# Performance work log

Hardware: AMD Instinct MI355X
Metric: run time of the kernel (lower is better)

## Reference

```python
import jax, jax.numpy as jnp
import numpy as np

TOKENS = 50257
DIMS = 1024
BATCH = 4
SEQ = 4096


def setup_inputs() -> dict:
    key = jax.random.key(0)
    k1, k2 = jax.random.split(key)
    x = jax.random.randint(k1, (BATCH, SEQ), 0, TOKENS, dtype=jnp.int64 if jax.config.jax_enable_x64 else jnp.int32)
    # nn.Linear(tokens, dims).weight has shape [dims, tokens]
    W = jax.random.normal(k2, (DIMS, TOKENS), dtype=jnp.float32) * (1.0 / np.sqrt(TOKENS))
    return {"x": x, "W": W}


def reference(x, W):
    # Original: out = one_hot(x, tokens) @ W.T  (Linear with no bias).
    # one_hot @ W.T is mathematically a row gather from W.T: out[b, s, :] = W[:, x[b, s]].
    # We compute the identical result without materializing the [B, S, tokens] one-hot.
    return jnp.take(W.T, x, axis=0)  # [B, S, dims]
```

## Files before the change

kernel.cpp:

```cpp
#include <hip/hip_runtime.h>


#define DIMS    1024
#define TOKENS  50257
#define WBITS   6
#define WSIZE   64
#define NW      ((TOKENS + WSIZE - 1) / WSIZE)

__global__ void zero_cnt(int* cnt) {
    int t = threadIdx.x;
    if (t < NW) cnt[t] = 0;
}

__global__ void hist_kernel(const int* __restrict__ x, int* __restrict__ cnt, int n) {
    int i = blockIdx.x * blockDim.x + threadIdx.x;
    if (i < n) atomicAdd(&cnt[x[i] >> WBITS], 1);
}

__global__ __launch_bounds__(1024) void scan_kernel(const int* __restrict__ cnt,
                                                    int* __restrict__ offs,
                                                    int* __restrict__ cursor) {
    __shared__ int s[1024];
    int t = threadIdx.x;
    int v = (t < NW) ? cnt[t] : 0;
    s[t] = v;
    __syncthreads();
    for (int off = 1; off < 1024; off <<= 1) {
        int u = (t >= off) ? s[t - off] : 0;
        __syncthreads();
        s[t] += u;
        __syncthreads();
    }
    if (t < NW) {
        offs[t + 1] = s[t];
        cursor[t]   = s[t] - v;
    }
    if (t == 0) offs[0] = 0;
}

__global__ void scatter_kernel(const int* __restrict__ x, int* __restrict__ cursor,
                               int* __restrict__ sorted_pos, int* __restrict__ sorted_tok,
                               int n) {
    int i = blockIdx.x * blockDim.x + threadIdx.x;
    if (i < n) {
        int tok = x[i];
        int p = atomicAdd(&cursor[tok >> WBITS], 1);
        sorted_pos[p] = i;
        sorted_tok[p] = tok;
    }
}

__global__ __launch_bounds__(256) void embed_main(
    const float* __restrict__ W,
    const int* __restrict__ offs,
    const int* __restrict__ sorted_pos,
    const int* __restrict__ sorted_tok,
    float* __restrict__ out)
{
    __shared__ float tile[WSIZE * 65];
    const int w     = blockIdx.x;
    const int dbase = blockIdx.y * WSIZE;
    const int t  = threadIdx.x;
    const int c  = t & 63;
    const int rq = t >> 6;

    const int id0 = w * WSIZE;
    const int id  = id0 + c;
    const bool ok = (id < TOKENS);

    #pragma unroll
    for (int i = 0; i < 16; ++i) {
        int r = i * 4 + rq;
        float v = ok ? W[(size_t)(dbase + r) * TOKENS + id] : 0.0f;
        tile[r * 65 + c] = v;
    }
    __syncthreads();

    const int beg = offs[w];
    const int n   = offs[w + 1] - beg;
    const int d  = t & 63;
    const int jo = t >> 6;
    for (int jb = 0; jb < n; jb += 4) {
        int j = jb + jo;
        if (j < n) {
            int tok = sorted_tok[beg + j];
            int p   = sorted_pos[beg + j];
            float v = tile[d * 65 + (tok - id0)];
            out[(size_t)p * DIMS + dbase + d] = v;
        }
    }
}

extern "C" void kernel_launch(void* const* d_in, const int* in_sizes, int n_in,
                              void* d_out, int out_size, void* d_ws, size_t ws_size,
                              hipStream_t stream) {
    const int*   x = (const int*)d_in[0];
    const float* W = (const float*)d_in[1];
    float*     out = (float*)d_out;

    const int n = in_sizes[0];

    int* cnt        = (int*)d_ws;
    int* offs       = cnt + NW;
    int* cursor     = offs + (NW + 1);
    int* sorted_pos = cursor + NW;
    int* sorted_tok = sorted_pos + n;

    zero_cnt<<<1, 1024, 0, stream>>>(cnt);
    hist_kernel<<<(n + 255) / 256, 256, 0, stream>>>(x, cnt, n);
    scan_kernel<<<1, 1024, 0, stream>>>(cnt, offs, cursor);
    scatter_kernel<<<(n + 255) / 256, 256, 0, stream>>>(x, cursor, sorted_pos, sorted_tok, n);

    dim3 grid(NW, DIMS / WSIZE);
    embed_main<<<grid, 256, 0, stream>>>(W, offs, sorted_pos, sorted_tok, out);
}
```

Baseline: 345.2 us.

## Fuse bucket sort into one block kernel and widen embed tiles to 128

Replaces the four preprocessing launches (zero, histogram, scan, scatter) with a single 1024-thread block that stages x in LDS, bins with shared atomics, scans and scatters. Sorted entries are packed as position<<16|token in one 32-bit word. The transpose tile grows from 64x64 to 128x128 with 512 threads per block, which halves the number of column windows. Packing assumes positions fit in 16 bits; n=16384 does fit. The single-block sort serialises work on one CU, and the larger tile raises LDS use to about 66KB per block, which may lower occupancy.

```diff
diff --git a/kernel.cpp b/kernel.cpp
--- a/kernel.cpp
+++ b/kernel.cpp
@@ -3,90 +3,92 @@
 
 #define DIMS    1024
 #define TOKENS  50257
-#define WBITS   6
-#define WSIZE   64
+#define WBITS   7
+#define WSIZE   128
 #define NW      ((TOKENS + WSIZE - 1) / WSIZE)
+#define PAD     129
+#define NMAX    16384
 
-__global__ void zero_cnt(int* cnt) {
-    int t = threadIdx.x;
-    if (t < NW) cnt[t] = 0;
-}
+__global__ __launch_bounds__(1024) void sort_kernel(
+    const int* __restrict__ x, int n,
+    int* __restrict__ offs,
+    unsigned int* __restrict__ sorted)
+{
+    __shared__ int xl[NMAX];
+    __shared__ int bins[NW];
+    __shared__ int scanbuf[512];
+    __shared__ int cursor[NW];
+    const int t = threadIdx.x;
 
-__global__ void hist_kernel(const int* __restrict__ x, int* __restrict__ cnt, int n) {
-    int i = blockIdx.x * blockDim.x + threadIdx.x;
-    if (i < n) atomicAdd(&cnt[x[i] >> WBITS], 1);
-}
+    const bool fits = (n <= NMAX);
+    if (fits) for (int i = t; i < n; i += 1024) xl[i] = x[i];
+    if (t < NW) bins[t] = 0;
+    __syncthreads();
+    const int* xs = fits ? xl : x;
 
-__global__ __launch_bounds__(1024) void scan_kernel(const int* __restrict__ cnt,
-                                                    int* __restrict__ offs,
-                                                    int* __restrict__ cursor) {
-    __shared__ int s[1024];
-    int t = threadIdx.x;
-    int v = (t < NW) ? cnt[t] : 0;
-    s[t] = v;
+    for (int i = t; i < n; i += 1024)
+        atomicAdd(&bins[xs[i] >> WBITS], 1);
     __syncthreads();
-    for (int off = 1; off < 1024; off <<= 1) {
-        int u = (t >= off) ? s[t - off] : 0;
+
+    if (t < 512) scanbuf[t] = (t < NW) ? bins[t] : 0;
+    __syncthreads();
+    for (int off = 1; off < 512; off <<= 1) {
+        int u = 0;
+        if (t < 512 && t >= off) u = scanbuf[t - off];
         __syncthreads();
-        s[t] += u;
+        if (t < 512) scanbuf[t] += u;
         __syncthreads();
     }
     if (t < NW) {
-        offs[t + 1] = s[t];
-        cursor[t]   = s[t] - v;
+        offs[t + 1] = scanbuf[t];
+        cursor[t]   = scanbuf[t] - bins[t];
     }
     if (t == 0) offs[0] = 0;
-}
+    __syncthreads();
 
-__global__ void scatter_kernel(const int* __restrict__ x, int* __restrict__ cursor,
-                               int* __restrict__ sorted_pos, int* __restrict__ sorted_tok,
-                               int n) {
-    int i = blockIdx.x * blockDim.x + threadIdx.x;
-    if (i < n) {
-        int tok = x[i];
+    for (int i = t; i < n; i += 1024) {
+        int tok = xs[i];
         int p = atomicAdd(&cursor[tok >> WBITS], 1);
-        sorted_pos[p] = i;
-        sorted_tok[p] = tok;
+        sorted[p] = ((unsigned int)i << 16) | (unsigned int)tok;
     }
 }
 
-__global__ __launch_bounds__(256) void embed_main(
+__global__ __launch_bounds__(512) void embed_main(
     const float* __restrict__ W,
     const int* __restrict__ offs,
-    const int* __restrict__ sorted_pos,
-    const int* __restrict__ sorted_tok,
+    const unsigned int* __restrict__ sorted,
     float* __restrict__ out)
 {
-    __shared__ float tile[WSIZE * 65];
+    __shared__ float tile[WSIZE * PAD];
     const int w     = blockIdx.x;
     const int dbase = blockIdx.y * WSIZE;
-    const int t  = threadIdx.x;
-    const int c  = t & 63;
-    const int rq = t >> 6;
+    const int t     = threadIdx.x;
+    const int id0   = w << WBITS;
 
-    const int id0 = w * WSIZE;
-    const int id  = id0 + c;
-    const bool ok = (id < TOKENS);
+    const int beg = offs[w];
+    const int nn  = offs[w + 1] - beg;
 
-    #pragma unroll
-    for (int i = 0; i < 16; ++i) {
-        int r = i * 4 + rq;
-        float v = ok ? W[(size_t)(dbase + r) * TOKENS + id] : 0.0f;
-        tile[r * 65 + c] = v;
+    const int c  = t & 127;
+    const int r0 = t >> 7;
+    const int id = id0 + c;
+    if (id < TOKENS) {
+        #pragma unroll
+        for (int i = 0; i < 32; ++i) {
+            int r = (i << 2) + r0;
+            tile[r * PAD + c] = W[(size_t)(dbase + r) * TOKENS + id];
+        }
     }
     __syncthreads();
 
-    const int beg = offs[w];
-    const int n   = offs[w + 1] - beg;
-    const int d  = t & 63;
-    const int jo = t >> 6;
-    for (int jb = 0; jb < n; jb += 4) {
+    const int d  = t & 127;
+    const int jo = t >> 7;
+    for (int jb = 0; jb < nn; jb += 4) {
         int j = jb + jo;
-        if (j < n) {
-            int tok = sorted_tok[beg + j];
-            int p   = sorted_pos[beg + j];
-            float v = tile[d * 65 + (tok - id0)];
-            out[(size_t)p * DIMS + dbase + d] = v;
+        if (j < nn) {
+            unsigned int v = sorted[beg + j];
+            int p   = (int)(v >> 16);
+            int col = (int)(v & 0xFFFFu) - id0;
+            out[(size_t)p * DIMS + dbase + d] = tile[d * PAD + col];
         }
     }
 }
@@ -100,17 +102,11 @@
 
     const int n = in_sizes[0];
 
-    int* cnt        = (int*)d_ws;
-    int* offs       = cnt + NW;
-    int* cursor     = offs + (NW + 1);
-    int* sorted_pos = cursor + NW;
-    int* sorted_tok = sorted_pos + n;
+    int* offs              = (int*)d_ws;
+    unsigned int* sorted   = (unsigned int*)(offs + (NW + 1));
 
-    zero_cnt<<<1, 1024, 0, stream>>>(cnt);
-    hist_kernel<<<(n + 255) / 256, 256, 0, stream>>>(x, cnt, n);
-    scan_kernel<<<1, 1024, 0, stream>>>(cnt, offs, cursor);
-    scatter_kernel<<<(n + 255) / 256, 256, 0, stream>>>(x, cursor, sorted_pos, sorted_tok, n);
+    sort_kernel<<<1, 1024, 0, stream>>>(x, n, offs, sorted);
 
     dim3 grid(NW, DIMS / WSIZE);
-    embed_main<<<grid, 256, 0, stream>>>(W, offs, sorted_pos, sorted_tok, out);
+    embed_main<<<grid, 512, 0, stream>>>(W, offs, sorted, out);
 }
```

After: 325.0 us. 5.8% less time.
